# Performance work log

Hardware: AMD Instinct MI355X
Metric: run time of the kernel (lower is better)

The kernel has to match this reference:

```python
import jax, jax.numpy as jnp
from jax import lax
import numpy as np

B, T, C, N = 64, 1024, 1, 128  # batch, max seq len, num_conjugates, num_tags


def setup_inputs() -> dict:
    key = jax.random.key(0)
    ks = jax.random.split(key, 6)
    emissions = jax.random.normal(ks[0], (B, T, C, N), dtype=jnp.float32)
    token_sizes = jax.random.randint(ks[1], (B,), T // 2, T + 1)  # ragged lengths in [512, 1024]
    targets = jax.random.randint(ks[2], (B, T), 0, N)
    transitions = jax.random.normal(ks[3], (1, C, N, N), dtype=jnp.float32) * 0.1
    head_transitions = jax.random.normal(ks[4], (1, C, N), dtype=jnp.float32) * 0.1
    last_transitions = jax.random.normal(ks[5], (1, C, N), dtype=jnp.float32) * 0.1
    return dict(emissions=emissions, token_sizes=token_sizes, targets=targets,
                transitions=transitions, head_transitions=head_transitions,
                last_transitions=last_transitions)


def _crf(emissions, token_sizes, targets, transitions, head_transitions, last_transitions):
    # emissions: [B, T, C, N] padded; token_sizes: [B]; targets: [B, T]
    Bq, Tq, Cq, Nq = emissions.shape
    trans = transitions[0]          # [C, N, N]
    head = head_transitions[0]      # [C, N]
    last = last_transitions[0]      # [C, N]

    # ---- log partition (Log semiring forward algorithm; same math as the
    # log-depth semiring tree reduction in crf_partition) ----
    alpha0 = head[None, :, :] + emissions[:, 0]            # [B, C, N]
    emits = jnp.moveaxis(emissions[:, 1:], 1, 0)           # [T-1, B, C, N]
    valid = jnp.arange(1, Tq)[:, None] < token_sizes[None, :]  # [T-1, B]

    def step(alpha, inp):
        emit_t, v = inp
        # alpha[b,c,i] + trans[c,i,j] -> logsumexp over i
        new = jax.nn.logsumexp(alpha[:, :, :, None] + trans[None], axis=2) + emit_t
        return jnp.where(v[:, None, None], new, alpha), None

    alphaT, _ = lax.scan(step, alpha0, (emits, valid))
    log_partitions = jax.nn.logsumexp(alphaT + last[None, :, :], axis=-1)  # [B, C]

    # ---- path score (crf_segment_reduce with Log semiring) ----
    emit_sel = jnp.take_along_axis(emissions, targets[:, :, None, None], axis=3)[..., 0]  # [B, T, C]
    mask = (jnp.arange(Tq)[None, :] < token_sizes[:, None]).astype(emissions.dtype)       # [B, T]
    emit_sum = jnp.sum(emit_sel * mask[:, :, None], axis=1)                               # [B, C]

    prev_t, curr_t = targets[:, :-1], targets[:, 1:]
    trans_sel = trans[:, prev_t, curr_t]                                                  # [C, B, T-1]
    mask2 = (jnp.arange(1, Tq)[None, :] < token_sizes[:, None]).astype(emissions.dtype)   # [B, T-1]
    trans_sum = jnp.sum(trans_sel * mask2[None], axis=-1)                                 # [C, B]

    head_sel = head[:, targets[:, 0]]                                                     # [C, B]
    last_tag = jnp.take_along_axis(targets, (token_sizes - 1)[:, None], axis=1)[:, 0]     # [B]
    last_sel = last[:, last_tag]                                                          # [C, B]

    log_scores = emit_sum + trans_sum.T + head_sel.T + last_sel.T                         # [B, C]
    return jnp.stack([log_partitions, log_scores])  # [2, B, C]


def reference(emissions, token_sizes, targets, transitions, head_transitions, last_transitions):
    return _crf(emissions, token_sizes, targets, transitions, head_transitions, last_transitions)
```

## Files before the change

kernel.cpp:

```cpp
#include <hip/hip_runtime.h>
#include <math.h>

#define Bq 64
#define Tq 1024
#define Nq 128
#define SEG 129
#define NFW (SEG - 1)
#define NBW (SEG - 1)
#define WPC 16
#define LN2 0.6931471805599453f

typedef __attribute__((ext_vector_type(8))) _Float16 half8;
typedef __attribute__((ext_vector_type(2))) _Float16 h2;
typedef __attribute__((ext_vector_type(4))) float f32x4;

union BU { int u[4]; int4 v; half8 h; };

__device__ __forceinline__ int pk16(float a, float b) {
    auto p = __builtin_amdgcn_cvt_pkrtz(a, b);
    return *(int*)&p;
}

__device__ __forceinline__ int MMAP(int q, int g, int j) {
    return 16 * (2 * q + (j >> 2)) + 4 * g + (j & 3);
}

__device__ __forceinline__ int4 packRowQ(const float* __restrict__ bp, int q, int g) {
    const float4 x = *(const float4*)(bp + 32*q + 4*g);
    const float4 y = *(const float4*)(bp + 32*q + 16 + 4*g);
    return make_int4(pk16(__expf(x.x), __expf(x.y)),
                     pk16(__expf(x.z), __expf(x.w)),
                     pk16(__expf(y.x), __expf(y.y)),
                     pk16(__expf(y.z), __expf(y.w)));
}

__global__ __launch_bounds__(256)
void crf_prep_kernel(const float* __restrict__ trans,
                     int4* __restrict__ aF, int4* __restrict__ aB) {
    const int fb = blockIdx.x;
    const bool fwd = (fb < 8);
    const int kf = (fb & 7) * 4 + (threadIdx.x >> 6);
    const int L = threadIdx.x & 63;
    const int c = L & 15, g = L >> 4;
    const int r = kf >> 2, q = kf & 3;
    BU v;
    #pragma unroll
    for (int j = 0; j < 8; ++j) {
        const int m = MMAP(q, g, j);
        const int n = 16 * r + c;
        const float tv = fwd ? trans[m * Nq + n] : trans[n * Nq + m];
        v.h[j] = (_Float16)__expf(tv);
    }
    (fwd ? aF : aB)[kf * 64 + L] = v.v;
}

__device__ __forceinline__ void ustep(
    int k, int lenc, int L,
    const int4 (&eeL)[8][4][64],
    const half8 (&afrag)[32], BU (&bf)[4], int& Ecum)
{
    BU ee[4], beff[4];
    #pragma unroll
    for (int q = 0; q < 4; ++q) ee[q].v = eeL[k - 1][q][L];
    #pragma unroll
    for (int q = 0; q < 4; ++q) beff[q].h = bf[q].h * ee[q].h;
    f32x4 acc[8];
    #pragma unroll
    for (int r = 0; r < 8; ++r) {
        f32x4 z = {0.f, 0.f, 0.f, 0.f};
        z = __builtin_amdgcn_mfma_f32_16x16x32_f16(afrag[r*4+0], beff[0].h, z, 0, 0, 0);
        z = __builtin_amdgcn_mfma_f32_16x16x32_f16(afrag[r*4+1], beff[1].h, z, 0, 0, 0);
        z = __builtin_amdgcn_mfma_f32_16x16x32_f16(afrag[r*4+2], beff[2].h, z, 0, 0, 0);
        z = __builtin_amdgcn_mfma_f32_16x16x32_f16(afrag[r*4+3], beff[3].h, z, 0, 0, 0);
        acc[r] = z;
    }
    float mx = 0.f;
    #pragma unroll
    for (int r = 0; r < 8; ++r) {
        #pragma unroll
        for (int i = 0; i < 4; ++i) mx = fmaxf(mx, acc[r][i]);
    }
    mx = fmaxf(mx, __shfl_xor(mx, 16, 64));
    mx = fmaxf(mx, __shfl_xor(mx, 32, 64));
    const int eb = (__float_as_int(mx) >> 23) & 255;
    const float sig = __int_as_float((253 - eb) << 23);
    const bool act = (k <= lenc);
    #pragma unroll
    for (int q = 0; q < 4; ++q) {
        const int n0 = pk16(acc[2*q][0]*sig,   acc[2*q][1]*sig);
        const int n1 = pk16(acc[2*q][2]*sig,   acc[2*q][3]*sig);
        const int n2 = pk16(acc[2*q+1][0]*sig, acc[2*q+1][1]*sig);
        const int n3 = pk16(acc[2*q+1][2]*sig, acc[2*q+1][3]*sig);
        bf[q].u[0] = act ? n0 : bf[q].u[0];
        bf[q].u[1] = act ? n1 : bf[q].u[1];
        bf[q].u[2] = act ? n2 : bf[q].u[2];
        bf[q].u[3] = act ? n3 : bf[q].u[3];
    }
    Ecum += act ? (eb - 126) : 0;
}

__global__ __launch_bounds__(64, 1)
void crf_worker_kernel(const float* __restrict__ emissions,
                       const int4* __restrict__ aF,
                       const int4* __restrict__ aB,
                       const int* __restrict__ token_sizes,
                       const float* __restrict__ head,
                       const float* __restrict__ last,
                       float* __restrict__ wsA, float* __restrict__ wsB,
                       float* __restrict__ wsLa, float* __restrict__ wsLb) {
    const int L = threadIdx.x;
    const int bid = blockIdx.x;

    __shared__ __align__(16) int4 eeL[8][4][64];

    const int b = bid >> 4;
    const int wv = bid & 15;
    const bool isFwd = (wv < 8);
    const int half_ = wv & 7;
    const int c = L & 15;
    const int g = L >> 4;
    const int s = (isFwd ? 1 : 2) + 16 * half_ + c;

    const float* em_c = emissions + (size_t)b * Tq * Nq;
    const int tsz = token_sizes[b];
    const int nst = tsz - 1;
    const int base = nst / SEG;
    const int rem = nst % SEG;
    const int lo = 1 + (s - 1) * base + min(s - 1, rem);
    const int lenc = base + ((s <= rem) ? 1 : 0);
    const int hi = lo + lenc - 1;
    const int kmax = base + 1;

    half8 afrag[32];
    {
        const int4* asrc = isFwd ? aF : aB;
        #pragma unroll
        for (int kf = 0; kf < 32; ++kf) {
            BU t; t.v = asrc[kf * 64 + L];
            afrag[kf] = t.h;
        }
    }

    BU bf[4];
    float M0c;
    {
        float a0[32];
        float mx = -1e30f;
        #pragma unroll
        for (int q = 0; q < 4; ++q) {
            #pragma unroll
            for (int j2 = 0; j2 < 8; ++j2) {
                const int m = MMAP(q, g, j2);
                float v;
                if (isFwd) v = (s == 1)   ? (head[m] + em_c[m]) : 0.f;
                else       v = (s == SEG) ? last[m]             : 0.f;
                a0[q*8+j2] = v;
                mx = fmaxf(mx, v);
            }
        }
        mx = fmaxf(mx, __shfl_xor(mx, 16, 64));
        mx = fmaxf(mx, __shfl_xor(mx, 32, 64));
        M0c = mx;
        #pragma unroll
        for (int q = 0; q < 4; ++q) {
            #pragma unroll
            for (int p = 0; p < 4; ++p)
                bf[q].u[p] = pk16(__expf(a0[q*8+2*p]   - M0c),
                                  __expf(a0[q*8+2*p+1] - M0c));
        }
    }

    BU eeHi[4];
    if (isFwd) {
        const int one2 = pk16(1.0f, 1.0f);
        const int4 ones = make_int4(one2, one2, one2, one2);
        #pragma unroll
        for (int q = 0; q < 4; ++q) eeL[0][q][L] = ones;
        #pragma unroll
        for (int i = 1; i < 8; ++i) {
            const int row = min(lo + i - 1, hi - 1);
            const float* bp = em_c + (size_t)row * Nq;
            #pragma unroll
            for (int q = 0; q < 4; ++q) eeL[i][q][L] = packRowQ(bp, q, g);
        }
        const float* bp = em_c + (size_t)hi * Nq;
        #pragma unroll
        for (int q = 0; q < 4; ++q) eeHi[q].v = packRowQ(bp, q, g);
    } else {
        #pragma unroll
        for (int i = 0; i < 8; ++i) {
            const int row = max(hi - i, lo);
            const float* bp = em_c + (size_t)row * Nq;
            #pragma unroll
            for (int q = 0; q < 4; ++q) eeL[i][q][L] = packRowQ(bp, q, g);
        }
    }
    __syncthreads();

    int Ecum = 0;
    ustep(1, lenc, L, eeL, afrag, bf, Ecum);
    ustep(2, lenc, L, eeL, afrag, bf, Ecum);
    ustep(3, lenc, L, eeL, afrag, bf, Ecum);
    ustep(4, lenc, L, eeL, afrag, bf, Ecum);
    if (kmax >= 5) ustep(5, lenc, L, eeL, afrag, bf, Ecum);
    if (kmax >= 6) ustep(6, lenc, L, eeL, afrag, bf, Ecum);
    if (kmax >= 7) ustep(7, lenc, L, eeL, afrag, bf, Ecum);
    if (kmax >= 8) ustep(8, lenc, L, eeL, afrag, bf, Ecum);

    {
        float* dst = isFwd ? (wsA + ((size_t)(s - 1) * Bq + b) * Nq)
                           : (wsB + ((size_t)(s - 2) * Bq + b) * Nq);
        #pragma unroll
        for (int q = 0; q < 4; ++q) {
            f32x4 v0, v1;
            #pragma unroll
            for (int t = 0; t < 4; ++t) {
                float m0 = isFwd ? (float)eeHi[q].h[t]     : 1.0f;
                float m1 = isFwd ? (float)eeHi[q].h[4 + t] : 1.0f;
                v0[t] = (float)bf[q].h[t]     * m0;
                v1[t] = (float)bf[q].h[4 + t] * m1;
            }
            *(f32x4*)(dst + 32*q + 4*g)      = v0;
            *(f32x4*)(dst + 32*q + 16 + 4*g) = v1;
        }
        if (g == 0) {
            const float led = M0c + (float)Ecum * LN2;
            if (isFwd) wsLa[(s - 1) * Bq + b] = led;
            else       wsLb[(s - 2) * Bq + b] = led;
        }
    }
}

__global__ __launch_bounds__(1024)
void crf_combine_kernel(const float* __restrict__ wsA,
                        const float* __restrict__ wsB,
                        const float* __restrict__ wsLa,
                        const float* __restrict__ wsLb,
                        const float* __restrict__ emissions,
                        const int* __restrict__ token_sizes,
                        const int* __restrict__ targets,
                        const float* __restrict__ transitions,
                        const float* __restrict__ head,
                        const float* __restrict__ last,
                        float* __restrict__ out) {
    const int bid = blockIdx.x;
    const int tid = threadIdx.x;
    __shared__ float part[16];

    if (bid < Bq) {
        const int chain = bid;
        const int wq = tid >> 6;
        const int l = tid & 63;
        float tot = 0.f;
        #pragma unroll
        for (int rep = 0; rep < 8; ++rep) {
            const int j = wq + 16 * rep;
            const float* bb = wsB + ((size_t)j * Bq + chain) * Nq;
            const float* aa = wsA + ((size_t)j * Bq + chain) * Nq;
            float z = bb[l] * aa[l] + bb[l + 64] * aa[l + 64];
            float cc = bb[l] + bb[l + 64];
            #pragma unroll
            for (int off = 32; off >= 1; off >>= 1) {
                z  += __shfl_xor(z, off, 64);
                cc += __shfl_xor(cc, off, 64);
            }
            float term = __logf(z) + wsLa[j * Bq + chain];
            term += (j == NFW - 1) ? wsLb[(NBW - 1) * Bq + chain] : -__logf(cc);
            tot += term;
        }
        if (l == 0) part[wq] = tot;
        __syncthreads();
        if (tid == 0) {
            float tz = 0.f;
            #pragma unroll
            for (int i = 0; i < 16; ++i) tz += part[i];
            out[chain] = tz;
        }
        return;
    }
    {
        const int b = bid - Bq;
        const int tsz = token_sizes[b];
        const int* tg = targets + b * Tq;
        const float* emc = emissions + (size_t)b * Tq * Nq;
        float sc = 0.f;
        if (tid < tsz) {
            const int cur = tg[tid];
            sc = emc[(size_t)tid * Nq + cur];
            if (tid >= 1) sc += transitions[tg[tid - 1] * Nq + cur];
        }
        #pragma unroll
        for (int off = 32; off >= 1; off >>= 1)
            sc += __shfl_xor(sc, off, 64);
        if ((tid & 63) == 0) part[tid >> 6] = sc;
        __syncthreads();
        if (tid == 0) {
            float tot = 0.f;
            #pragma unroll
            for (int i = 0; i < 16; ++i) tot += part[i];
            out[Bq + b] = tot + head[tg[0]] + last[tg[tsz - 1]];
        }
    }
}

extern "C" void kernel_launch(void* const* d_in, const int* in_sizes, int n_in,
                              void* d_out, int out_size, void* d_ws, size_t ws_size,
                              hipStream_t stream) {
    const float* emissions   = (const float*)d_in[0];
    const int*   token_sizes = (const int*)d_in[1];
    const int*   targets     = (const int*)d_in[2];
    const float* transitions = (const float*)d_in[3];
    const float* head        = (const float*)d_in[4];
    const float* last        = (const float*)d_in[5];
    float* out = (float*)d_out;

    char* wp = (char*)d_ws;
    int4* aF = (int4*)wp;                                wp += 32 * 64 * 16;
    int4* aB = (int4*)wp;                                wp += 32 * 64 * 16;
    float* wsA  = (float*)wp;                            wp += (size_t)NFW * Bq * Nq * 4;
    float* wsB  = (float*)wp;                            wp += (size_t)NBW * Bq * Nq * 4;
    float* wsLa = (float*)wp;                            wp += NFW * Bq * 4;
    float* wsLb = (float*)wp;                            wp += NBW * Bq * 4;

    crf_prep_kernel<<<16, 256, 0, stream>>>(transitions, aF, aB);
    crf_worker_kernel<<<Bq * WPC, 64, 0, stream>>>(
        emissions, aF, aB, token_sizes, head, last,
        wsA, wsB, wsLa, wsLb);
    crf_combine_kernel<<<2 * Bq, 1024, 0, stream>>>(
        wsA, wsB, wsLa, wsLb,
        emissions, token_sizes, targets, transitions, head, last, out);
}
```

Measured before the change: 36.92 us.

## Share emission tiles between paired forward/backward waves in one block

Pairs a forward and a backward wave in a single 128-thread block covering the same 16 segments. The two waves cooperatively load each segment's emission rows into shared memory once, instead of each wave loading its own set. Backward steps index the shared tile in reverse, and the forward epilogue reads its last emission row from shared memory. This halves redundant global emission loads and block count (576 blocks vs 1024), at the cost of a few idle lanes at the edges and a block-wide barrier coupling the two waves.

Result: no change. 36.49 us (-1.1%).

```diff
diff --git a/kernel.cpp b/kernel.cpp
--- a/kernel.cpp
+++ b/kernel.cpp
@@ -7,7 +7,7 @@
 #define SEG 129
 #define NFW (SEG - 1)
 #define NBW (SEG - 1)
-#define WPC 16
+#define BPC 9
 #define LN2 0.6931471805599453f
 
 typedef __attribute__((ext_vector_type(8))) _Float16 half8;
@@ -54,16 +54,22 @@
     (fwd ? aF : aB)[kf * 64 + L] = v.v;
 }
 
-__device__ __forceinline__ void ustep(
-    int k, int lenc, int L,
+__device__ __forceinline__ void pstep(
+    int k, int lenc, int eeIdx, bool useEE, int L,
     const int4 (&eeL)[8][4][64],
     const half8 (&afrag)[32], BU (&bf)[4], int& Ecum)
 {
-    BU ee[4], beff[4];
-    #pragma unroll
-    for (int q = 0; q < 4; ++q) ee[q].v = eeL[k - 1][q][L];
-    #pragma unroll
-    for (int q = 0; q < 4; ++q) beff[q].h = bf[q].h * ee[q].h;
+    BU beff[4];
+    if (useEE) {
+        #pragma unroll
+        for (int q = 0; q < 4; ++q) {
+            BU e; e.v = eeL[eeIdx][q][L];
+            beff[q].h = bf[q].h * e.h;
+        }
+    } else {
+        #pragma unroll
+        for (int q = 0; q < 4; ++q) beff[q] = bf[q];
+    }
     f32x4 acc[8];
     #pragma unroll
     for (int r = 0; r < 8; ++r) {
@@ -99,7 +105,7 @@
     Ecum += act ? (eb - 126) : 0;
 }
 
-__global__ __launch_bounds__(64, 1)
+__global__ __launch_bounds__(128, 1)
 void crf_worker_kernel(const float* __restrict__ emissions,
                        const int4* __restrict__ aF,
                        const int4* __restrict__ aB,
@@ -108,18 +114,21 @@
                        const float* __restrict__ last,
                        float* __restrict__ wsA, float* __restrict__ wsB,
                        float* __restrict__ wsLa, float* __restrict__ wsLb) {
-    const int L = threadIdx.x;
-    const int bid = blockIdx.x;
-
-    __shared__ __align__(16) int4 eeL[8][4][64];
-
-    const int b = bid >> 4;
-    const int wv = bid & 15;
-    const bool isFwd = (wv < 8);
-    const int half_ = wv & 7;
+    const int tid = threadIdx.x;
+    const int L = tid & 63;
+    const int w01 = tid >> 6;
     const int c = L & 15;
     const int g = L >> 4;
-    const int s = (isFwd ? 1 : 2) + 16 * half_ + c;
+    const int bid = blockIdx.x;
+    const int b = bid / BPC;
+    const int wg = bid % BPC;
+
+    __shared__ __align__(16) int4 eeL[8][4][64];
+
+    const int s_raw = 16 * wg + c + 1;
+    const int s = min(s_raw, SEG);
+    const bool isFwd = (w01 == 0);
+    const bool valid = isFwd ? (s_raw <= NFW) : (s_raw >= 2 && s_raw <= SEG);
 
     const float* em_c = emissions + (size_t)b * Tq * Nq;
     const int tsz = token_sizes[b];
@@ -141,6 +150,15 @@
         }
     }
 
+    #pragma unroll
+    for (int ii = 0; ii < 4; ++ii) {
+        const int i = 4 * w01 + ii;
+        const int row = min(lo + i, hi);
+        const float* bp = em_c + (size_t)row * Nq;
+        #pragma unroll
+        for (int q = 0; q < 4; ++q) eeL[i][q][L] = packRowQ(bp, q, g);
+    }
+
     BU bf[4];
     float M0c;
     {
@@ -152,8 +170,8 @@
             for (int j2 = 0; j2 < 8; ++j2) {
                 const int m = MMAP(q, g, j2);
                 float v;
-                if (isFwd) v = (s == 1)   ? (head[m] + em_c[m]) : 0.f;
-                else       v = (s == SEG) ? last[m]             : 0.f;
+                if (isFwd) v = (s_raw == 1)   ? (head[m] + em_c[m]) : 0.f;
+                else       v = (s_raw == SEG) ? last[m]             : 0.f;
                 a0[q*8+j2] = v;
                 mx = fmaxf(mx, v);
             }
@@ -170,53 +188,44 @@
         }
     }
 
-    BU eeHi[4];
+    __syncthreads();
+
+    int Ecum = 0;
     if (isFwd) {
-        const int one2 = pk16(1.0f, 1.0f);
-        const int4 ones = make_int4(one2, one2, one2, one2);
-        #pragma unroll
-        for (int q = 0; q < 4; ++q) eeL[0][q][L] = ones;
-        #pragma unroll
-        for (int i = 1; i < 8; ++i) {
-            const int row = min(lo + i - 1, hi - 1);
-            const float* bp = em_c + (size_t)row * Nq;
-            #pragma unroll
-            for (int q = 0; q < 4; ++q) eeL[i][q][L] = packRowQ(bp, q, g);
-        }
-        const float* bp = em_c + (size_t)hi * Nq;
-        #pragma unroll
-        for (int q = 0; q < 4; ++q) eeHi[q].v = packRowQ(bp, q, g);
+        pstep(1, lenc, 0,              false, L, eeL, afrag, bf, Ecum);
+        pstep(2, lenc, 0,              true,  L, eeL, afrag, bf, Ecum);
+        pstep(3, lenc, 1,              true,  L, eeL, afrag, bf, Ecum);
+        pstep(4, lenc, 2,              true,  L, eeL, afrag, bf, Ecum);
+        if (kmax >= 5) pstep(5, lenc, 3, true, L, eeL, afrag, bf, Ecum);
+        if (kmax >= 6) pstep(6, lenc, 4, true, L, eeL, afrag, bf, Ecum);
+        if (kmax >= 7) pstep(7, lenc, 5, true, L, eeL, afrag, bf, Ecum);
+        if (kmax >= 8) pstep(8, lenc, 6, true, L, eeL, afrag, bf, Ecum);
     } else {
-        #pragma unroll
-        for (int i = 0; i < 8; ++i) {
-            const int row = max(hi - i, lo);
-            const float* bp = em_c + (size_t)row * Nq;
-            #pragma unroll
-            for (int q = 0; q < 4; ++q) eeL[i][q][L] = packRowQ(bp, q, g);
-        }
-    }
-    __syncthreads();
-
-    int Ecum = 0;
-    ustep(1, lenc, L, eeL, afrag, bf, Ecum);
-    ustep(2, lenc, L, eeL, afrag, bf, Ecum);
-    ustep(3, lenc, L, eeL, afrag, bf, Ecum);
-    ustep(4, lenc, L, eeL, afrag, bf, Ecum);
-    if (kmax >= 5) ustep(5, lenc, L, eeL, afrag, bf, Ecum);
-    if (kmax >= 6) ustep(6, lenc, L, eeL, afrag, bf, Ecum);
-    if (kmax >= 7) ustep(7, lenc, L, eeL, afrag, bf, Ecum);
-    if (kmax >= 8) ustep(8, lenc, L, eeL, afrag, bf, Ecum);
-
-    {
+        pstep(1, lenc, max(lenc - 1, 0), true, L, eeL, afrag, bf, Ecum);
+        pstep(2, lenc, max(lenc - 2, 0), true, L, eeL, afrag, bf, Ecum);
+        pstep(3, lenc, max(lenc - 3, 0), true, L, eeL, afrag, bf, Ecum);
+        pstep(4, lenc, max(lenc - 4, 0), true, L, eeL, afrag, bf, Ecum);
+        if (kmax >= 5) pstep(5, lenc, max(lenc - 5, 0), true, L, eeL, afrag, bf, Ecum);
+        if (kmax >= 6) pstep(6, lenc, max(lenc - 6, 0), true, L, eeL, afrag, bf, Ecum);
+        if (kmax >= 7) pstep(7, lenc, max(lenc - 7, 0), true, L, eeL, afrag, bf, Ecum);
+        if (kmax >= 8) pstep(8, lenc, max(lenc - 8, 0), true, L, eeL, afrag, bf, Ecum);
+    }
+
+    if (valid) {
         float* dst = isFwd ? (wsA + ((size_t)(s - 1) * Bq + b) * Nq)
                            : (wsB + ((size_t)(s - 2) * Bq + b) * Nq);
+        BU eeHi[4];
+        if (isFwd) {
+            #pragma unroll
+            for (int q = 0; q < 4; ++q) eeHi[q].v = eeL[lenc - 1][q][L];
+        }
         #pragma unroll
         for (int q = 0; q < 4; ++q) {
             f32x4 v0, v1;
             #pragma unroll
             for (int t = 0; t < 4; ++t) {
-                float m0 = isFwd ? (float)eeHi[q].h[t]     : 1.0f;
-                float m1 = isFwd ? (float)eeHi[q].h[4 + t] : 1.0f;
+                const float m0 = isFwd ? (float)eeHi[q].h[t]     : 1.0f;
+                const float m1 = isFwd ? (float)eeHi[q].h[4 + t] : 1.0f;
                 v0[t] = (float)bf[q].h[t]     * m0;
                 v1[t] = (float)bf[q].h[4 + t] * m1;
             }
@@ -323,7 +332,7 @@
     float* wsLb = (float*)wp;                            wp += NBW * Bq * 4;
 
     crf_prep_kernel<<<16, 256, 0, stream>>>(transitions, aF, aB);
-    crf_worker_kernel<<<Bq * WPC, 64, 0, stream>>>(
+    crf_worker_kernel<<<Bq * BPC, 128, 0, stream>>>(
         emissions, aF, aB, token_sizes, head, last,
         wsA, wsB, wsLa, wsLb);
     crf_combine_kernel<<<2 * Bq, 1024, 0, stream>>>(
```
